# Kernel optimization log

Hardware: AMD Instinct MI355X
Metric: run time of the kernel (lower is better)

The kernel has to match this reference:

```python
import jax, jax.numpy as jnp
import numpy as np

H, D = 8, 32            # num_heads, per-head out_dim (same for C1/C2/C3/state)
ALPHA = 0.2             # leaky-relu negative slope
N_C, N_S = 10000, 1024  # nodes per C type, state nodes
E_CC, E_CS = 120000, 10000
IN_C, IN_S = 128, 64


def setup_inputs() -> dict:
    key = jax.random.key(0)
    ks = jax.random.split(key, 20)
    xn = lambda k, sh, s=1.0: jax.random.normal(k, sh, dtype=jnp.float32) * s
    inp = {}
    inp["feat_C1"] = xn(ks[0], (N_C, IN_C))
    inp["feat_C2"] = xn(ks[1], (N_C, IN_C))
    inp["feat_C3"] = xn(ks[2], (N_C, IN_C))
    inp["feat_state"] = xn(ks[3], (N_S, IN_S))
    # linear weights (xavier-ish scale) and zero biases
    inp["W_node"] = xn(ks[4], (3, IN_C, H * D), 0.06)
    inp["b_node"] = jnp.zeros((3, H * D), jnp.float32)
    inp["W_cc"] = xn(ks[5], (9, IN_C, H * D), 0.06)
    inp["b_cc"] = jnp.zeros((9, H * D), jnp.float32)
    inp["W_cs"] = xn(ks[6], (3, IN_C, H * D), 0.06)
    inp["b_cs"] = jnp.zeros((3, H * D), jnp.float32)
    inp["W_in"] = xn(ks[7], (IN_S, H * D), 0.08)
    inp["b_in"] = jnp.zeros((H * D,), jnp.float32)
    # attention vectors: [..., 0] = src vec, [..., 1] = dst vec
    inp["attn_cc"] = xn(ks[8], (9, 2, H, D), 0.3)
    inp["attn_cs"] = xn(ks[9], (3, 2, H, D), 0.3)
    # edge lists; relation r = 3*src_type + dst_type for cc
    inp["edges_cc_src"] = jax.random.randint(ks[10], (9, E_CC), 0, N_C, dtype=jnp.int32)
    inp["edges_cc_dst"] = jax.random.randint(ks[11], (9, E_CC), 0, N_C, dtype=jnp.int32)
    inp["edges_cs_src"] = jax.random.randint(ks[12], (3, E_CS), 0, N_C, dtype=jnp.int32)
    inp["edges_cs_dst"] = jax.random.randint(ks[13], (3, E_CS), 0, N_S, dtype=jnp.int32)
    return inp


def _segment_softmax(e, dst, n):
    # e: [E, H]; softmax over edges sharing the same dst node (DGL edge_softmax)
    m = jax.ops.segment_max(e, dst, num_segments=n)
    ex = jnp.exp(e - m[dst])
    s = jax.ops.segment_sum(ex, dst, num_segments=n)
    return ex / s[dst]


def _gat_relation(Wh_src, Wh_dst_self, a_src_vec, a_dst_vec, src, dst, n_dst):
    # Wh_src: [Ns,H,D] projected src feats for this relation
    # Wh_dst_self: [Nd,H,D] dst-type self projection (used for dst attention)
    a_s = jnp.sum(Wh_src * a_src_vec, axis=-1)       # [Ns,H]
    a_d = jnp.sum(Wh_dst_self * a_dst_vec, axis=-1)  # [Nd,H]
    e = jax.nn.leaky_relu(a_s[src] + a_d[dst], ALPHA)   # [E,H]
    a = _segment_softmax(e, dst, n_dst)                 # [E,H]
    msg = Wh_src[src] * a[:, :, None]                   # [E,H,D]
    return jax.ops.segment_sum(msg, dst, num_segments=n_dst)


def _forward(feat_C1, feat_C2, feat_C3, feat_state, W_node, b_node, W_cc, b_cc,
             W_cs, b_cs, W_in, b_in, attn_cc, attn_cs,
             edges_cc_src, edges_cc_dst, edges_cs_src, edges_cs_dst):
    feats_c = [feat_C1, feat_C2, feat_C3]
    n_c = [f.shape[0] for f in feats_c]
    # self projections (used as dst attention features)
    Wh_node = [(feats_c[t] @ W_node[t] + b_node[t]).reshape(-1, H, D) for t in range(3)]
    out_c = [jnp.zeros_like(Wh_node[t]) for t in range(3)]
    # 9 C->C relations: r = 3*s + d
    for r in range(9):
        s, d = divmod(r, 3)
        Wh = (feats_c[s] @ W_cc[r] + b_cc[r]).reshape(-1, H, D)
        ft = _gat_relation(Wh, Wh_node[d], attn_cc[r, 0], attn_cc[r, 1],
                           edges_cc_src[r], edges_cc_dst[r], n_c[d])
        out_c[d] = out_c[d] + ft
    # state: 'in' self projection + 3 C->state relations
    Wh_in = (feat_state @ W_in + b_in).reshape(-1, H, D)
    out_s = Wh_in
    n_s = feat_state.shape[0]
    for t in range(3):
        Wh = (feats_c[t] @ W_cs[t] + b_cs[t]).reshape(-1, H, D)
        ft = _gat_relation(Wh, Wh_in, attn_cs[t, 0], attn_cs[t, 1],
                           edges_cs_src[t], edges_cs_dst[t], n_s)
        out_s = out_s + ft
    relu = jax.nn.relu
    return (relu(out_c[0]), relu(out_c[1]), relu(out_c[2]), relu(out_s))


def reference(feat_C1, feat_C2, feat_C3, feat_state, W_node, b_node, W_cc, b_cc,
              W_cs, b_cs, W_in, b_in, attn_cc, attn_cs,
              edges_cc_src, edges_cc_dst, edges_cs_src, edges_cs_dst):
    return _forward(feat_C1, feat_C2, feat_C3, feat_state, W_node, b_node, W_cc,
                    b_cc, W_cs, b_cs, W_in, b_in, attn_cc, attn_cs,
                    edges_cc_src, edges_cc_dst, edges_cs_src, edges_cs_dst)
```

## Files before the change

### kernel.cpp

```cpp
#include <hip/hip_runtime.h>


#define H_ 8
#define D_ 32
#define HD 256
#define NC 10000
#define NS 1024
#define INC 128
#define INS 64
#define ECC 120000
#define ECS 10000
#define ALPHA 0.2f
#define CAP 64

typedef unsigned short u16;
typedef __attribute__((ext_vector_type(8))) short short8;
typedef __attribute__((ext_vector_type(4))) float f32x4;

static constexpr size_t WHB_CC = 0;
static constexpr size_t WHB_CS = 23040000;
static constexpr size_t WHB_IN = 30720000;
static constexpr size_t FB0  = 15491072;
static constexpr size_t ASCC = FB0;
static constexpr size_t ADCC = FB0 + 720000;
static constexpr size_t ASCS = FB0 + 1440000;
static constexpr size_t ADCS = FB0 + 1680000;
static constexpr size_t BAF  = FB0 + 1704576;
static constexpr size_t FBC  = 34437760;
static constexpr size_t FBS  = 38277760;
static constexpr size_t WTCC = 38343296;
static constexpr size_t WTCS = 38638208;
static constexpr size_t WTIN = 38736512;
static constexpr size_t WAT  = 38752896;
static constexpr size_t IBYTE = 77768704;
static constexpr size_t SBYTE = 78140992;

static constexpr int TOTE  = 9 * ECC + 3 * ECS;
static constexpr int NB_Z0 = 91;
static constexpr int NB_FT = 3814;
static constexpr int NB_WT = 104;
static constexpr int NB_FO = 32;
static constexpr int NB_K2 = 2710;

__device__ __forceinline__ u16 f2b(float f) {
  unsigned u = __float_as_uint(f);
  return (u16)((u + 0x7FFFu + ((u >> 16) & 1u)) >> 16);
}
__device__ __forceinline__ float bl(unsigned u) { return __uint_as_float(u << 16); }
__device__ __forceinline__ float bh(unsigned u) { return __uint_as_float(u & 0xffff0000u); }

__global__ __launch_bounds__(256) void k_prep(
    const float* f1, const float* f2, const float* f3, const float* fs,
    const float* Wcc, const float* Wcs, const float* Win, const float* Wnode,
    const float* bcc, const float* bnode, const float* bcs, const float* bin,
    const float* accv, const float* acsv,
    u16* wsu, float* wsf, int* cnts) {
  __shared__ float Ls[64 * 65];
  int b = blockIdx.x, t = threadIdx.x;
  if (b < NB_Z0) {
    int i = b * 256 + t;
    if (i < 23268) ((int4*)cnts)[i] = make_int4(0, 0, 0, 0);
    return;
  }
  b -= NB_Z0;
  if (b < NB_FT) {
    const float* src; u16* dst; int idx, n4;
    if (b < 3750) {
      int ty = b / 1250;
      src = (ty == 0) ? f1 : (ty == 1) ? f2 : f3;
      dst = wsu + FBC + (size_t)ty * 1280000;
      idx = (b - ty * 1250) * 256 + t; n4 = 320000;
    } else {
      src = fs; dst = wsu + FBS; idx = (b - 3750) * 256 + t; n4 = 16384;
    }
    if (idx < n4) {
      float4 v = ((const float4*)src)[idx];
      uint2 o;
      o.x = (unsigned)f2b(v.x) | ((unsigned)f2b(v.y) << 16);
      o.y = (unsigned)f2b(v.z) | ((unsigned)f2b(v.w) << 16);
      *(uint2*)(dst + (size_t)idx * 4) = o;
    }
    return;
  }
  b -= NB_FT;
  if (b < NB_WT) {
    int mat = b >> 3, sub = b & 7;
    int K = (mat == 12) ? INS : INC;
    if (mat == 12 && sub >= 4) return;
    int k0 = (sub >> 2) * 64, n0 = (sub & 3) * 64;
    const float* src; u16* dst;
    if (mat < 9)        { src = Wcc + (size_t)mat * INC * HD;        dst = wsu + WTCC + (size_t)mat * 32768; }
    else if (mat < 12)  { src = Wcs + (size_t)(mat - 9) * INC * HD;  dst = wsu + WTCS + (size_t)(mat - 9) * 32768; }
    else                { src = Win;                                 dst = wsu + WTIN; }
    #pragma unroll
    for (int it = 0; it < 4; it++) {
      int idx = t + it * 256;
      int r = idx >> 4, c4 = idx & 15;
      float4 v = *(const float4*)&src[(size_t)(k0 + r) * HD + n0 + c4 * 4];
      Ls[r * 65 + c4 * 4 + 0] = v.x; Ls[r * 65 + c4 * 4 + 1] = v.y;
      Ls[r * 65 + c4 * 4 + 2] = v.z; Ls[r * 65 + c4 * 4 + 3] = v.w;
    }
    __syncthreads();
    int n = t >> 2, k8 = (t & 3) * 16;
    unsigned o[8];
    #pragma unroll
    for (int j = 0; j < 8; j++) {
      u16 lo = f2b(Ls[(k8 + 2 * j) * 65 + n]);
      u16 hi = f2b(Ls[(k8 + 2 * j + 1) * 65 + n]);
      o[j] = (unsigned)lo | ((unsigned)hi << 16);
    }
    uint4* dp = (uint4*)&dst[(size_t)(n0 + n) * K + k0 + k8];
    dp[0] = make_uint4(o[0], o[1], o[2], o[3]);
    dp[1] = make_uint4(o[4], o[5], o[6], o[7]);
    return;
  }
  b -= NB_WT;
  int tile = b >> 3, sub = b & 7;
  int K = (tile == 3) ? INS : INC;
  int c0 = sub * 8;
  for (int idx = t; idx < 8 * K; idx += 256) {
    int col = c0 + idx / K, k = idx % K;
    int m = col >> 3, h = col & 7;
    const float* W = nullptr; const float* av = nullptr;
    if (tile < 3) {
      if (m < 3)      { int r = 3*tile + m; W = Wcc + (size_t)r*INC*HD;   av = accv + (size_t)r*512 + h*32; }
      else if (m < 6) { int r = 3*(m-3) + tile; W = Wnode + (size_t)tile*INC*HD; av = accv + (size_t)r*512 + 256 + h*32; }
      else if (m == 6){ W = Wcs + (size_t)tile*INC*HD; av = acsv + (size_t)tile*512 + h*32; }
    } else if (m < 3) { W = Win; av = acsv + (size_t)m*512 + 256 + h*32; }
    float s = 0.f;
    if (W) {
      const float* wp = W + (size_t)k * HD + h * 32;
      #pragma unroll 8
      for (int d = 0; d < 32; d++) s += wp[d] * av[d];
    }
    wsu[WAT + (size_t)tile * 8192 + (size_t)col * K + k] = f2b(s);
  }
  if (sub == 0 && t < 64) {
    int col = t, m = col >> 3, h = col & 7;
    const float* bb = nullptr; const float* av = nullptr;
    if (tile < 3) {
      if (m < 3)      { int r = 3*tile + m; bb = bcc + (size_t)r*HD;  av = accv + (size_t)r*512 + h*32; }
      else if (m < 6) { int r = 3*(m-3) + tile; bb = bnode + (size_t)tile*HD; av = accv + (size_t)r*512 + 256 + h*32; }
      else if (m == 6){ bb = bcs + (size_t)tile*HD; av = acsv + (size_t)tile*512 + h*32; }
    } else if (m < 3) { bb = bin; av = acsv + (size_t)m*512 + 256 + h*32; }
    float s = 0.f;
    if (bb) for (int d = 0; d < 32; d++) s += bb[h*32 + d] * av[d];
    wsf[BAF + tile * 64 + col] = s;
  }
}

__global__ __launch_bounds__(256, 2) void k_fuse(
    u16* wsu, float* wsf, const float* bcc, const float* bcs, const float* bin,
    const int* eccs, const int* eccd, const int* ecss, const int* ecsd,
    int* cnts, u16* slt) {
  __shared__ __align__(16) char smem[69632];
  int gb = blockIdx.x, t = threadIdx.x;
  if ((gb % 5) == 4) {
    int k = gb / 5;
    int i0 = (k * 256 + t) * 8;
    if (i0 >= TOTE) return;
    int dd[8], ss[8], p[8];
    int cbase;
    if (i0 < 9 * ECC) {
      int r = i0 / ECC;
      int4 d0 = *(const int4*)&eccd[i0]; int4 d1 = *(const int4*)&eccd[i0 + 4];
      int4 s0 = *(const int4*)&eccs[i0]; int4 s1 = *(const int4*)&eccs[i0 + 4];
      dd[0]=d0.x; dd[1]=d0.y; dd[2]=d0.z; dd[3]=d0.w;
      dd[4]=d1.x; dd[5]=d1.y; dd[6]=d1.z; dd[7]=d1.w;
      ss[0]=s0.x; ss[1]=s0.y; ss[2]=s0.z; ss[3]=s0.w;
      ss[4]=s1.x; ss[5]=s1.y; ss[6]=s1.z; ss[7]=s1.w;
      cbase = r * NC;
    } else {
      int u0 = i0 - 9 * ECC;
      int r = u0 / ECS;
      int4 d0 = *(const int4*)&ecsd[u0]; int4 d1 = *(const int4*)&ecsd[u0 + 4];
      int4 s0 = *(const int4*)&ecss[u0]; int4 s1 = *(const int4*)&ecss[u0 + 4];
      dd[0]=d0.x; dd[1]=d0.y; dd[2]=d0.z; dd[3]=d0.w;
      dd[4]=d1.x; dd[5]=d1.y; dd[6]=d1.z; dd[7]=d1.w;
      ss[0]=s0.x; ss[1]=s0.y; ss[2]=s0.z; ss[3]=s0.w;
      ss[4]=s1.x; ss[5]=s1.y; ss[6]=s1.z; ss[7]=s1.w;
      cbase = 90000 + r * NS;
    }
    #pragma unroll
    for (int q = 0; q < 8; q++) p[q] = atomicAdd(&cnts[cbase + dd[q]], 1);
    #pragma unroll
    for (int q = 0; q < 8; q++)
      if (p[q] < CAP) slt[((size_t)(cbase + dd[q])) * CAP + p[q]] = (u16)ss[q];
    return;
  }
  int g = 4 * (gb / 5) + (gb % 5);
  if (g >= 2157) return;
  u16* As = (u16*)smem;
  u16* Bs = (u16*)(smem + 34816);
  const u16 *A, *Bt; const float* bias = nullptr; u16* C = nullptr;
  int M, K, r0, n0 = 0, ty = 0;
  bool isScore = false;
  if (g < 1896) {
    int z = g / 158, rem = g - z * 158;
    int by = rem / 79, bx = rem - by * 79;
    r0 = bx * 128; n0 = by * 128; M = NC; K = 128;
    if (z < 9) { A = wsu + FBC + (size_t)(z/3)*1280000; Bt = wsu + WTCC + (size_t)z*32768; bias = bcc + (size_t)z*HD; C = wsu + WHB_CC + (size_t)z*NC*HD; }
    else { int q = z - 9; A = wsu + FBC + (size_t)q*1280000; Bt = wsu + WTCS + (size_t)q*32768; bias = bcs + (size_t)q*HD; C = wsu + WHB_CS + (size_t)q*NC*HD; }
  } else if (g < 1912) {
    int loc = g - 1896; int by = loc / 8, bx = loc - by * 8;
    r0 = bx * 128; n0 = by * 128; M = NS; K = 64;
    A = wsu + FBS; Bt = wsu + WTIN; bias = bin; C = wsu + WHB_IN;
  } else if (g < 2149) {
    isScore = true; ty = (g - 1912) / 79; int bx = (g - 1912) % 79;
    r0 = bx * 128; M = NC; K = 128;
    A = wsu + FBC + (size_t)ty * 1280000; Bt = wsu + WAT + (size_t)ty * 8192;
  } else {
    isScore = true; ty = 3; int bx = g - 2149;
    r0 = bx * 128; M = NS; K = 64;
    A = wsu + FBS; Bt = wsu + WAT + (size_t)3 * 8192;
  }
  int SA = K + 8;
  int NB = isScore ? 64 : 128;
  {
    int ksh = (K == 128) ? 4 : 3;
    int kmask = (1 << ksh) - 1;
    int sc8 = SA >> 3;
    const uint4* ga = (const uint4*)(A + (size_t)r0 * K);
    const uint4* gb2 = (const uint4*)(Bt + (size_t)n0 * K);
    uint4* la = (uint4*)As; uint4* lb = (uint4*)Bs;
    int tota = (128 * K) >> 3, totb = (NB * K) >> 3;
    for (int i = t; i < tota; i += 256) la[(i >> ksh) * sc8 + (i & kmask)] = ga[i];
    for (int i = t; i < totb; i += 256) lb[(i >> ksh) * sc8 + (i & kmask)] = gb2[i];
  }
  __syncthreads();
  int lane = t & 63, w = t >> 6, l16 = lane & 15, quad = lane >> 4;
  int arow0 = w * 32 + l16;
  if (!isScore) {
    f32x4 acc[2][8];
    #pragma unroll
    for (int i = 0; i < 2; i++)
      #pragma unroll
      for (int j = 0; j < 8; j++) acc[i][j] = (f32x4){0.f, 0.f, 0.f, 0.f};
    for (int ks = 0; ks < K; ks += 32) {
      int ko = ks + quad * 8;
      short8 a0 = *(const short8*)&As[(size_t)arow0 * SA + ko];
      short8 a1 = *(const short8*)&As[(size_t)(arow0 + 16) * SA + ko];
      #pragma unroll
      for (int j = 0; j < 8; j++) {
        short8 bfr = *(const short8*)&Bs[(size_t)(j * 16 + l16) * SA + ko];
        acc[0][j] = __builtin_amdgcn_mfma_f32_16x16x32_bf16(a0, bfr, acc[0][j], 0, 0, 0);
        acc[1][j] = __builtin_amdgcn_mfma_f32_16x16x32_bf16(a1, bfr, acc[1][j], 0, 0, 0);
      }
    }
    __syncthreads();
    float* Cl = (float*)smem;
    #pragma unroll
    for (int i = 0; i < 2; i++) {
      int rl0 = w * 32 + i * 16 + quad * 4;
      #pragma unroll
      for (int j = 0; j < 8; j++) {
        int cl = j * 16 + l16;
        float bv = bias[n0 + cl];
        #pragma unroll
        for (int rg = 0; rg < 4; rg++)
          Cl[(rl0 + rg) * 132 + cl] = acc[i][j][rg] + bv;
      }
    }
    __syncthreads();
    for (int task = t; task < 2048; task += 256) {
      int row = task >> 4, seg = task & 15;
      int gr = r0 + row;
      if (gr >= M) continue;
      const float* cp = Cl + row * 132 + seg * 8;
      float4 v0 = *(const float4*)cp;
      float4 v1 = *(const float4*)(cp + 4);
      uint4 o;
      o.x = (unsigned)f2b(v0.x) | ((unsigned)f2b(v0.y) << 16);
      o.y = (unsigned)f2b(v0.z) | ((unsigned)f2b(v0.w) << 16);
      o.z = (unsigned)f2b(v1.x) | ((unsigned)f2b(v1.y) << 16);
      o.w = (unsigned)f2b(v1.z) | ((unsigned)f2b(v1.w) << 16);
      *(uint4*)&C[(size_t)gr * HD + n0 + seg * 8] = o;
    }
  } else {
    f32x4 acc[2][4];
    #pragma unroll
    for (int i = 0; i < 2; i++)
      #pragma unroll
      for (int j = 0; j < 4; j++) acc[i][j] = (f32x4){0.f, 0.f, 0.f, 0.f};
    for (int ks = 0; ks < K; ks += 32) {
      int ko = ks + quad * 8;
      short8 a0 = *(const short8*)&As[(size_t)arow0 * SA + ko];
      short8 a1 = *(const short8*)&As[(size_t)(arow0 + 16) * SA + ko];
      #pragma unroll
      for (int j = 0; j < 4; j++) {
        short8 bfr = *(const short8*)&Bs[(size_t)(j * 16 + l16) * SA + ko];
        acc[0][j] = __builtin_amdgcn_mfma_f32_16x16x32_bf16(a0, bfr, acc[0][j], 0, 0, 0);
        acc[1][j] = __builtin_amdgcn_mfma_f32_16x16x32_bf16(a1, bfr, acc[1][j], 0, 0, 0);
      }
    }
    float* sp[4]; float bav[4];
    #pragma unroll
    for (int j = 0; j < 4; j++) {
      int col = j * 16 + l16;
      int m = col >> 3, h = col & 7;
      float* p = nullptr;
      if (ty < 3) {
        if (m < 3)       p = wsf + ASCC + (size_t)(3*ty + m) * NC * H_;
        else if (m < 6)  p = wsf + ADCC + (size_t)(3*(m-3) + ty) * NC * H_;
        else if (m == 6) p = wsf + ASCS + (size_t)ty * NC * H_;
      } else if (m < 3)  p = wsf + ADCS + (size_t)m * NS * H_;
      sp[j] = p ? (p + h) : nullptr;
      bav[j] = wsf[BAF + ty * 64 + col];
    }
    #pragma unroll
    for (int i = 0; i < 2; i++) {
      int rl0 = w * 32 + i * 16 + quad * 4;
      #pragma unroll
      for (int j = 0; j < 4; j++) {
        if (!sp[j]) continue;
        #pragma unroll
        for (int rg = 0; rg < 4; rg++) {
          int gr = r0 + rl0 + rg;
          if (gr < M) sp[j][(size_t)gr * 8] = acc[i][j][rg] + bav[j];
        }
      }
    }
  }
}

__global__ __launch_bounds__(256) void k_agg(const u16* wsu, const float* wsf,
                                             const int* cnts, const u16* slt,
                                             float* out) {
  int t = threadIdx.x, lane = t & 63, w = t >> 6;
  int node = blockIdx.x * 4 + w;
  int sub = lane & 31, half = lane >> 5, h = sub >> 2;
  float acc[8] = {0.f, 0.f, 0.f, 0.f, 0.f, 0.f, 0.f, 0.f};
  bool isC = node < 3 * NC;
  int dtype = 0, n;
  if (isC) { dtype = node / NC; n = node - dtype * NC; } else { n = node - 3 * NC; }
  for (int j = 0; j < 3; j++) {
    int cidx; const float* ASp; float adn; const u16* whb;
    if (isC) {
      int r = j * 3 + dtype;
      cidx = r * NC + n;
      ASp  = wsf + ASCC + (size_t)r * NC * H_;
      adn  = wsf[ADCC + (size_t)r * NC * H_ + (size_t)n * H_ + h];
      whb  = wsu + WHB_CC + (size_t)r * NC * HD;
    } else {
      int r = j;
      cidx = 90000 + r * NS + n;
      ASp  = wsf + ASCS + (size_t)r * NC * H_;
      adn  = wsf[ADCS + (size_t)r * NS * H_ + (size_t)n * H_ + h];
      whb  = wsu + WHB_CS + (size_t)r * NC * HD;
    }
    int cnt = cnts[cidx];
    cnt = min(cnt, CAP);
    if (cnt <= 0) continue;
    int vsrc = ((int)slt[(size_t)cidx * CAP + min(lane, cnt - 1)]) << 5;
    const char* sb_ = (const char*)ASp + h * 4;
    const char* wb_ = (const char*)whb + sub * 16;
    float a8[8] = {0.f, 0.f, 0.f, 0.f, 0.f, 0.f, 0.f, 0.f};
    float sH = 0.f;
    for (int e = 0; e < cnt; e += 4) {
      int i0 = min(e + half, cnt - 1);
      int i1 = min(e + 2 + half, cnt - 1);
      int so0 = __shfl(vsrc, i0);
      int so1 = __shfl(vsrc, i1);
      float sc0 = *(const float*)(sb_ + so0) + adn;
      float sc1 = *(const float*)(sb_ + so1) + adn;
      uint4 m0 = *(const uint4*)(wb_ + ((size_t)so0 << 4));
      uint4 m1 = *(const uint4*)(wb_ + ((size_t)so1 << 4));
      sc0 = fmaxf(sc0, ALPHA * sc0);
      sc1 = fmaxf(sc1, ALPHA * sc1);
      float w0 = (e + half < cnt) ? __expf(sc0) : 0.f;
      float w1 = (e + 2 + half < cnt) ? __expf(sc1) : 0.f;
      a8[0] += w0 * bl(m0.x); a8[1] += w0 * bh(m0.x);
      a8[2] += w0 * bl(m0.y); a8[3] += w0 * bh(m0.y);
      a8[4] += w0 * bl(m0.z); a8[5] += w0 * bh(m0.z);
      a8[6] += w0 * bl(m0.w); a8[7] += w0 * bh(m0.w);
      a8[0] += w1 * bl(m1.x); a8[1] += w1 * bh(m1.x);
      a8[2] += w1 * bl(m1.y); a8[3] += w1 * bh(m1.y);
      a8[4] += w1 * bl(m1.z); a8[5] += w1 * bh(m1.z);
      a8[6] += w1 * bl(m1.w); a8[7] += w1 * bh(m1.w);
      sH += w0 + w1;
    }
    sH += __shfl_xor(sH, 32);
    float inv = 1.f / sH;
    #pragma unroll
    for (int q = 0; q < 8; q++) acc[q] += a8[q] * inv;
  }
  #pragma unroll
  for (int q = 0; q < 8; q++) acc[q] += __shfl_xor(acc[q], 32);
  if (!isC) {
    uint4 m = *(const uint4*)((const char*)(wsu + WHB_IN) + (size_t)n * 512 + sub * 16);
    acc[0] += bl(m.x); acc[1] += bh(m.x); acc[2] += bl(m.y); acc[3] += bh(m.y);
    acc[4] += bl(m.z); acc[5] += bh(m.z); acc[6] += bl(m.w); acc[7] += bh(m.w);
  }
  float4 v;
  if (half == 0) v = make_float4(acc[0], acc[1], acc[2], acc[3]);
  else           v = make_float4(acc[4], acc[5], acc[6], acc[7]);
  v.x = fmaxf(v.x, 0.f); v.y = fmaxf(v.y, 0.f);
  v.z = fmaxf(v.z, 0.f); v.w = fmaxf(v.w, 0.f);
  *(float4*)(out + (size_t)node * HD + sub * 8 + half * 4) = v;
}

extern "C" void kernel_launch(void* const* d_in, const int* in_sizes, int n_in,
                              void* d_out, int out_size, void* d_ws, size_t ws_size,
                              hipStream_t stream) {
  (void)in_sizes; (void)n_in; (void)out_size; (void)ws_size;
  const float* f1    = (const float*)d_in[0];
  const float* f2    = (const float*)d_in[1];
  const float* f3    = (const float*)d_in[2];
  const float* fs    = (const float*)d_in[3];
  const float* Wnode = (const float*)d_in[4];
  const float* bnode = (const float*)d_in[5];
  const float* Wcc   = (const float*)d_in[6];
  const float* bcc   = (const float*)d_in[7];
  const float* Wcs   = (const float*)d_in[8];
  const float* bcs   = (const float*)d_in[9];
  const float* Win   = (const float*)d_in[10];
  const float* bin   = (const float*)d_in[11];
  const float* accv  = (const float*)d_in[12];
  const float* acsv  = (const float*)d_in[13];
  const int* eccs    = (const int*)d_in[14];
  const int* eccd    = (const int*)d_in[15];
  const int* ecss    = (const int*)d_in[16];
  const int* ecsd    = (const int*)d_in[17];
  float* wsf = (float*)d_ws;
  u16*   wsu = (u16*)d_ws;
  int*   cnts = (int*)((char*)d_ws + IBYTE);
  u16*   slt  = (u16*)((char*)d_ws + SBYTE);
  float* out = (float*)d_out;

  k_prep<<<dim3(NB_Z0 + NB_FT + NB_WT + NB_FO), 256, 0, stream>>>(
      f1, f2, f3, fs, Wcc, Wcs, Win, Wnode, bcc, bnode, bcs, bin, accv, acsv,
      wsu, wsf, cnts);
  k_fuse<<<dim3(NB_K2), 256, 0, stream>>>(
      wsu, wsf, bcc, bcs, bin, eccs, eccd, ecss, ecsd, cnts, slt);
  k_agg<<<dim3((3 * NC + NS) / 4), 256, 0, stream>>>(wsu, wsf, cnts, slt, out);
}
```

Measured before the change: 253.9 us.

## Restructure aggregation: whole-wave row gathers, batched edge weights, exp2 prescale

The aggregation kernel now has each lane own 4 output features of a 256-wide row. Each wave gathers a full source row per edge, 8 edges at a time, using readlane-broadcast source indices. Edge weights for the next 8 edges are computed one step ahead (8 edges × 8 heads across the wave) and broadcast via shuffles. The attention-score GEMM epilogue pre-multiplies by log2(e) so the kernel can use the hardware exp2 instead of expf. The aim is more coalesced gathers, no half-wave split and cross-half reductions, and better memory-level parallelism. The cost is more shuffles per edge and extra register pressure from 8 in-flight loads.

```diff
diff --git a/kernel.cpp b/kernel.cpp
--- a/kernel.cpp
+++ b/kernel.cpp
@@ -16,6 +16,7 @@
 typedef unsigned short u16;
 typedef __attribute__((ext_vector_type(8))) short short8;
 typedef __attribute__((ext_vector_type(4))) float f32x4;
+typedef __attribute__((ext_vector_type(2))) float f32x2;
 
 static constexpr size_t WHB_CC = 0;
 static constexpr size_t WHB_CS = 23040000;
@@ -316,7 +317,7 @@
         #pragma unroll
         for (int rg = 0; rg < 4; rg++) {
           int gr = r0 + rl0 + rg;
-          if (gr < M) sp[j][(size_t)gr * 8] = acc[i][j][rg] + bav[j];
+          if (gr < M) sp[j][(size_t)gr * 8] = (acc[i][j][rg] + bav[j]) * 1.44269504089f;
         }
       }
     }
@@ -328,75 +329,85 @@
                                              float* out) {
   int t = threadIdx.x, lane = t & 63, w = t >> 6;
   int node = blockIdx.x * 4 + w;
-  int sub = lane & 31, half = lane >> 5, h = sub >> 2;
-  float acc[8] = {0.f, 0.f, 0.f, 0.f, 0.f, 0.f, 0.f, 0.f};
+  int l3 = lane >> 3;
+  int h7 = lane & 7;
+  int lb = lane * 8;
+  f32x2 totA = {0.f, 0.f}, totB = {0.f, 0.f};
   bool isC = node < 3 * NC;
   int dtype = 0, n;
   if (isC) { dtype = node / NC; n = node - dtype * NC; } else { n = node - 3 * NC; }
   for (int j = 0; j < 3; j++) {
-    int cidx; const float* ASp; float adn; const u16* whb;
+    int cidx; const float* ASp; const float* ADp; const char* wb;
     if (isC) {
       int r = j * 3 + dtype;
       cidx = r * NC + n;
-      ASp  = wsf + ASCC + (size_t)r * NC * H_;
-      adn  = wsf[ADCC + (size_t)r * NC * H_ + (size_t)n * H_ + h];
-      whb  = wsu + WHB_CC + (size_t)r * NC * HD;
+      ASp = wsf + ASCC + (size_t)r * NC * H_;
+      ADp = wsf + ADCC + (size_t)r * NC * H_;
+      wb  = (const char*)(wsu + WHB_CC + (size_t)r * NC * HD);
     } else {
-      int r = j;
-      cidx = 90000 + r * NS + n;
-      ASp  = wsf + ASCS + (size_t)r * NC * H_;
-      adn  = wsf[ADCS + (size_t)r * NS * H_ + (size_t)n * H_ + h];
-      whb  = wsu + WHB_CS + (size_t)r * NC * HD;
-    }
-    int cnt = cnts[cidx];
-    cnt = min(cnt, CAP);
+      cidx = 90000 + j * NS + n;
+      ASp = wsf + ASCS + (size_t)j * NC * H_;
+      ADp = wsf + ADCS + (size_t)j * NS * H_;
+      wb  = (const char*)(wsu + WHB_CS + (size_t)j * NC * HD);
+    }
+    int cnt = min(cnts[cidx], CAP);
     if (cnt <= 0) continue;
-    int vsrc = ((int)slt[(size_t)cidx * CAP + min(lane, cnt - 1)]) << 5;
-    const char* sb_ = (const char*)ASp + h * 4;
-    const char* wb_ = (const char*)whb + sub * 16;
-    float a8[8] = {0.f, 0.f, 0.f, 0.f, 0.f, 0.f, 0.f, 0.f};
-    float sH = 0.f;
-    for (int e = 0; e < cnt; e += 4) {
-      int i0 = min(e + half, cnt - 1);
-      int i1 = min(e + 2 + half, cnt - 1);
-      int so0 = __shfl(vsrc, i0);
-      int so1 = __shfl(vsrc, i1);
-      float sc0 = *(const float*)(sb_ + so0) + adn;
-      float sc1 = *(const float*)(sb_ + so1) + adn;
-      uint4 m0 = *(const uint4*)(wb_ + ((size_t)so0 << 4));
-      uint4 m1 = *(const uint4*)(wb_ + ((size_t)so1 << 4));
-      sc0 = fmaxf(sc0, ALPHA * sc0);
-      sc1 = fmaxf(sc1, ALPHA * sc1);
-      float w0 = (e + half < cnt) ? __expf(sc0) : 0.f;
-      float w1 = (e + 2 + half < cnt) ? __expf(sc1) : 0.f;
-      a8[0] += w0 * bl(m0.x); a8[1] += w0 * bh(m0.x);
-      a8[2] += w0 * bl(m0.y); a8[3] += w0 * bh(m0.y);
-      a8[4] += w0 * bl(m0.z); a8[5] += w0 * bh(m0.z);
-      a8[6] += w0 * bl(m0.w); a8[7] += w0 * bh(m0.w);
-      a8[0] += w1 * bl(m1.x); a8[1] += w1 * bh(m1.x);
-      a8[2] += w1 * bl(m1.y); a8[3] += w1 * bh(m1.y);
-      a8[4] += w1 * bl(m1.z); a8[5] += w1 * bh(m1.z);
-      a8[6] += w1 * bl(m1.w); a8[7] += w1 * bh(m1.w);
-      sH += w0 + w1;
-    }
-    sH += __shfl_xor(sH, 32);
-    float inv = 1.f / sH;
-    #pragma unroll
-    for (int q = 0; q < 8; q++) acc[q] += a8[q] * inv;
-  }
-  #pragma unroll
-  for (int q = 0; q < 8; q++) acc[q] += __shfl_xor(acc[q], 32);
+    int srcid = (int)slt[(size_t)cidx * CAP + min(lane, cnt - 1)];
+    float adn = ADp[(size_t)n * H_ + h7];
+    f32x2 aA = {0.f, 0.f}, aB = {0.f, 0.f};
+    float zac = 0.f;
+    float wcur;
+    {
+      int ce = min(l3, cnt - 1);
+      int sid = __shfl(srcid, ce);
+      float sc = ASp[(size_t)sid * H_ + h7] + adn;
+      sc = fmaxf(sc, ALPHA * sc);
+      wcur = (l3 < cnt) ? __builtin_amdgcn_exp2f(sc) : 0.f;
+    }
+    for (int g = 0; g < cnt; g += 8) {
+      uint2 mreg[8];
+      #pragma unroll
+      for (int ee = 0; ee < 8; ee++) {
+        int ce = min(g + ee, cnt - 1);
+        int sre = __builtin_amdgcn_readlane(srcid, ce);
+        mreg[ee] = *(const uint2*)(wb + ((size_t)sre << 9) + lb);
+      }
+      float wold = wcur;
+      zac += wold;
+      if (g + 8 < cnt) {
+        int e = g + 8 + l3;
+        int ce = min(e, cnt - 1);
+        int sid = __shfl(srcid, ce);
+        float sc = ASp[(size_t)sid * H_ + h7] + adn;
+        sc = fmaxf(sc, ALPHA * sc);
+        wcur = (e < cnt) ? __builtin_amdgcn_exp2f(sc) : 0.f;
+      }
+      #pragma unroll
+      for (int ee = 0; ee < 8; ee++) {
+        float we = __shfl(wold, ee * 8 + l3);
+        f32x2 q0, q1;
+        q0.x = bl(mreg[ee].x); q0.y = bh(mreg[ee].x);
+        q1.x = bl(mreg[ee].y); q1.y = bh(mreg[ee].y);
+        aA += q0 * we;
+        aB += q1 * we;
+      }
+    }
+    zac += __shfl_xor(zac, 8);
+    zac += __shfl_xor(zac, 16);
+    zac += __shfl_xor(zac, 32);
+    float inv = 1.f / zac;
+    float invp = __shfl(inv, l3);
+    totA += aA * invp;
+    totB += aB * invp;
+  }
   if (!isC) {
-    uint4 m = *(const uint4*)((const char*)(wsu + WHB_IN) + (size_t)n * 512 + sub * 16);
-    acc[0] += bl(m.x); acc[1] += bh(m.x); acc[2] += bl(m.y); acc[3] += bh(m.y);
-    acc[4] += bl(m.z); acc[5] += bh(m.z); acc[6] += bl(m.w); acc[7] += bh(m.w);
-  }
-  float4 v;
-  if (half == 0) v = make_float4(acc[0], acc[1], acc[2], acc[3]);
-  else           v = make_float4(acc[4], acc[5], acc[6], acc[7]);
-  v.x = fmaxf(v.x, 0.f); v.y = fmaxf(v.y, 0.f);
-  v.z = fmaxf(v.z, 0.f); v.w = fmaxf(v.w, 0.f);
-  *(float4*)(out + (size_t)node * HD + sub * 8 + half * 4) = v;
+    uint2 m = *(const uint2*)((const char*)(wsu + WHB_IN) + (size_t)n * 512 + lb);
+    totA.x += bl(m.x); totA.y += bh(m.x);
+    totB.x += bl(m.y); totB.y += bh(m.y);
+  }
+  float4 v = make_float4(fmaxf(totA.x, 0.f), fmaxf(totA.y, 0.f),
+                         fmaxf(totB.x, 0.f), fmaxf(totB.y, 0.f));
+  *(float4*)(out + (size_t)node * HD + lane * 4) = v;
 }
 
 extern "C" void kernel_launch(void* const* d_in, const int* in_sizes, int n_in,
```

New measurement: 254.2 us. Within noise of the previous version (+0.1%).
